# Performance work log

Measured on AMD Instinct MI355X. Metric: run time of the kernel, lower is better.

## Reference

```python
import jax, jax.numpy as jnp
import numpy as np

N_NODES = 50000
N_EDGES = 800000
D = 64
NEG_SLOPE = 0.2


def setup_inputs() -> dict:
    key = jax.random.key(0)
    ks = jax.random.split(key, 16)
    inp = {
        "t": jnp.zeros((1,), jnp.float32),
        "x": jax.random.normal(ks[0], (N_NODES, D), jnp.float32),
        "edge_index": jax.random.randint(ks[1], (2, N_EDGES), 0, N_NODES, jnp.int64),
    }
    # 3 GATConv layers (64->64, 64->64, 64->64), heads=1
    s = 1.0 / np.sqrt(D)
    for li, k0 in zip((1, 2, 3), (2, 6, 10)):
        inp[f"W{li}"] = jax.random.normal(ks[k0], (D, D), jnp.float32) * s
        inp[f"a_src{li}"] = jax.random.normal(ks[k0 + 1], (D,), jnp.float32) * s
        inp[f"a_dst{li}"] = jax.random.normal(ks[k0 + 2], (D,), jnp.float32) * s
        inp[f"b{li}"] = jnp.zeros((D,), jnp.float32)
    return inp


def _gat_conv(x, src, dst, W, a_src, a_dst, b):
    # h = W x  (PyG: lin(x)), per-edge attention, segment softmax over dst
    n = x.shape[0]
    h = x @ W                                   # [N, D]
    score = jax.nn.leaky_relu(h[src] @ a_src + h[dst] @ a_dst, NEG_SLOPE)  # [E]
    smax = jax.ops.segment_max(score, dst, num_segments=n)                 # [N]
    ex = jnp.exp(score - smax[dst])                                        # [E]
    denom = jax.ops.segment_sum(ex, dst, num_segments=n)                   # [N]
    alpha = ex / denom[dst]                                                # [E]
    out = jax.ops.segment_sum(alpha[:, None] * h[src], dst, num_segments=n)
    return out + b


def reference(t, x, edge_index, W1, a_src1, a_dst1, b1, W2, a_src2, a_dst2, b2, W3, a_src3, a_dst3, b3):
    n = x.shape[0]
    # PyG GATConv default add_self_loops=True
    loops = jnp.arange(n, dtype=edge_index.dtype)
    src = jnp.concatenate([edge_index[0], loops])
    dst = jnp.concatenate([edge_index[1], loops])
    h = _gat_conv(x, src, dst, W1, a_src1, a_dst1, b1)
    h = jax.nn.relu(h)
    h = _gat_conv(h, src, dst, W2, a_src2, a_dst2, b2)
    h = jax.nn.relu(h)
    h = _gat_conv(h, src, dst, W3, a_src3, a_dst3, b3)
    return h
```

## Files before the change

kernel.cpp:

```cpp
#include <hip/hip_runtime.h>
#include <hip/hip_fp16.h>

#define NN 50000
#define NE 800000
#define D 64
#define GB ((NN + 63) / 64)
#define NBUCK ((NN + 127) >> 7)
#define CHUNK 4096
#define EBLKS ((NE + CHUNK - 1) / CHUNK)
#define CAPB 4096

__device__ __forceinline__ float lrelu(float s) { return (s > 0.0f) ? s : 0.2f * s; }


__global__ __launch_bounds__(256) void bin_pass(const int* __restrict__ ei,
                                                int* __restrict__ gcur,
                                                unsigned* __restrict__ pairs) {
  __shared__ int cnt_loc[NBUCK];
  __shared__ int base_loc[NBUCK];
  int t = threadIdx.x;
  int e0 = blockIdx.x * CHUNK;
  int n = (NE - e0 < CHUNK) ? (NE - e0) : CHUNK;
  for (int i = t; i < NBUCK; i += 256) cnt_loc[i] = 0;
  __syncthreads();
  for (int i = t; i < n; i += 256)
    atomicAdd(&cnt_loc[ei[NE + e0 + i] >> 7], 1);
  __syncthreads();
  for (int i = t; i < NBUCK; i += 256) {
    int c = cnt_loc[i];
    base_loc[i] = c ? (i * CAPB + atomicAdd(&gcur[i], c)) : 0;
    cnt_loc[i] = 0;
  }
  __syncthreads();
  for (int i = t; i < n; i += 256) {
    int src = ei[e0 + i];
    int dst = ei[NE + e0 + i];
    int b = dst >> 7;
    int off = atomicAdd(&cnt_loc[b], 1);
    unsigned pk = ((unsigned)src << 7) | (unsigned)(dst & 127);
    __builtin_nontemporal_store(pk, &pairs[base_loc[b] + off]);
  }
}

__global__ __launch_bounds__(256) void bucket_sort(const unsigned* __restrict__ pairs,
                                                   const int* __restrict__ gcur,
                                                   int* __restrict__ row_start,
                                                   int* __restrict__ deg,
                                                   int* __restrict__ sorted_src) {
  __shared__ int cnt[128];
  __shared__ int exc[128];
  __shared__ int cur[128];
  __shared__ int buf[CAPB];
  int b = blockIdx.x;
  int t = threadIdx.x;
  int n0 = b << 7;
  int start = b * CAPB;
  int cntb = gcur[b];
  if (cntb > CAPB) cntb = CAPB;
  if (t < 128) cnt[t] = 0;
  __syncthreads();
  for (int i = t; i < cntb; i += 256)
    atomicAdd(&cnt[pairs[start + i] & 127u], 1);
  __syncthreads();
  if (t < 128) exc[t] = cnt[t];
  __syncthreads();
  for (int s = 1; s < 128; s <<= 1) {
    int add = 0;
    if (t < 128 && t >= s) add = exc[t - s];
    __syncthreads();
    if (t < 128) exc[t] += add;
    __syncthreads();
  }
  if (t < 128) {
    int e = exc[t] - cnt[t];
    cur[t] = e;
    int nd = n0 + t;
    if (nd < NN) {
      row_start[nd] = start + e;
      deg[nd] = cnt[t];
    }
  }
  __syncthreads();
  for (int i = t; i < cntb; i += 256) {
    unsigned pk = pairs[start + i];
    int pos = atomicAdd(&cur[pk & 127u], 1);
    if (pos < CAPB) buf[pos] = (int)(pk >> 7);
  }
  __syncthreads();
  for (int i = t; i < cntb; i += 256)
    sorted_src[start + i] = buf[i];
}


__global__ __launch_bounds__(256) void gemm_feat(
    const float* __restrict__ xin, const float* __restrict__ W,
    const float* __restrict__ a_src, const float* __restrict__ a_dst,
    __half* __restrict__ h16, float* __restrict__ s_src, float* __restrict__ s_dst,
    int do_relu) {
  __shared__ float wlds[64 * 64];
  __shared__ float xT[64][68];
  __shared__ float psrc[64][17];
  __shared__ float pdst[64][17];
  int t = threadIdx.x;
  int n0 = blockIdx.x * 64;

  const float4* W4 = (const float4*)W;
  float4* wl4 = (float4*)wlds;
#pragma unroll
  for (int i = 0; i < 4; ++i) wl4[t + 256 * i] = W4[t + 256 * i];

#pragma unroll
  for (int i = 0; i < 4; ++i) {
    int idx = t + 256 * i;
    int r = idx >> 4, c4 = idx & 15;
    int n = n0 + r;
    float4 v = make_float4(0.f, 0.f, 0.f, 0.f);
    if (n < NN) v = ((const float4*)xin)[(size_t)n * 16 + c4];
    if (do_relu) {
      v.x = fmaxf(v.x, 0.f); v.y = fmaxf(v.y, 0.f);
      v.z = fmaxf(v.z, 0.f); v.w = fmaxf(v.w, 0.f);
    }
    xT[c4 * 4 + 0][r] = v.x;
    xT[c4 * 4 + 1][r] = v.y;
    xT[c4 * 4 + 2][r] = v.z;
    xT[c4 * 4 + 3][r] = v.w;
  }
  __syncthreads();

  int tr = t & 15, tc = t >> 4;
  float acc[4][4] = {};
#pragma unroll 8
  for (int k = 0; k < 64; ++k) {
    float4 xa = *(const float4*)&xT[k][tr * 4];
    float4 wv = *(const float4*)&wlds[k * 64 + tc * 4];
    float xs[4] = {xa.x, xa.y, xa.z, xa.w};
    float wj[4] = {wv.x, wv.y, wv.z, wv.w};
#pragma unroll
    for (int i = 0; i < 4; ++i)
#pragma unroll
      for (int j = 0; j < 4; ++j) acc[i][j] = fmaf(xs[i], wj[j], acc[i][j]);
  }

#pragma unroll
  for (int i = 0; i < 4; ++i) {
    int n = n0 + tr * 4 + i;
    if (n < NN) {
      __half2* dst = (__half2*)&h16[(size_t)n * 64 + tc * 4];
      dst[0] = __floats2half2_rn(acc[i][0], acc[i][1]);
      dst[1] = __floats2half2_rn(acc[i][2], acc[i][3]);
    }
  }

  float as[4], ad[4];
#pragma unroll
  for (int j = 0; j < 4; ++j) { as[j] = a_src[tc * 4 + j]; ad[j] = a_dst[tc * 4 + j]; }
#pragma unroll
  for (int i = 0; i < 4; ++i) {
    float p1 = 0.f, p2 = 0.f;
#pragma unroll
    for (int j = 0; j < 4; ++j) { p1 = fmaf(acc[i][j], as[j], p1); p2 = fmaf(acc[i][j], ad[j], p2); }
    psrc[tr * 4 + i][tc] = p1;
    pdst[tr * 4 + i][tc] = p2;
  }
  __syncthreads();
  if (t < 64) {
    int n = n0 + t;
    if (n < NN) {
      float s1 = 0.f, s2 = 0.f;
#pragma unroll
      for (int c = 0; c < 16; ++c) { s1 += psrc[t][c]; s2 += pdst[t][c]; }
      s_src[n] = s1;
      s_dst[n] = s2;
    }
  }
}

__global__ void agg_kernel(const int* __restrict__ sorted_src, const int* __restrict__ row_start,
                           const int* __restrict__ deg, const float* __restrict__ s_src,
                           const float* __restrict__ s_dst, const __half* __restrict__ h16,
                           const float* __restrict__ bias, float* __restrict__ out) {
  int gid = blockIdx.x * blockDim.x + threadIdx.x;
  int n = gid >> 5;
  if (n >= NN) return;
  int lane = threadIdx.x & 31;
  int start = row_start[n];
  int dg = deg[n];
  float sdn = s_dst[n];
  float sself = lrelu(s_src[n] + sdn);
  float exself = __expf(sself - 8.0f);

  float2 acc;
  {
    float2 f = __half22float2(*(const __half2*)&h16[(size_t)n * 64 + 2 * lane]);
    acc.x = exself * f.x;
    acc.y = exself * f.y;
  }
  float dpart = 0.0f;
  for (int base = 0; base < dg; base += 32) {
    int i = base + lane;
    bool act = (i < dg);
    int msrc = act ? __builtin_nontemporal_load(&sorted_src[start + i]) : 0;
    float s = act ? lrelu(s_src[msrc] + sdn) : -INFINITY;
    float ex = __expf(s - 8.0f);
    dpart += ex;
    int nch = (dg - base < 32) ? (dg - base) : 32;
    for (int b0 = 0; b0 < nch; b0 += 8) {
      float xs[8]; int ss[8]; unsigned vv[8];
#pragma unroll
      for (int e = 0; e < 8; ++e) {
        xs[e] = __shfl(ex, b0 + e, 32);
        ss[e] = __shfl(msrc, b0 + e, 32);
      }
#pragma unroll
      for (int e = 0; e < 8; ++e)
        vv[e] = *(const unsigned*)&h16[(size_t)ss[e] * 64 + 2 * lane];
#pragma unroll
      for (int e = 0; e < 8; ++e) {
        float2 f = __half22float2(*(__half2*)&vv[e]);
        acc.x = fmaf(xs[e], f.x, acc.x);
        acc.y = fmaf(xs[e], f.y, acc.y);
      }
    }
  }
#pragma unroll
  for (int off = 16; off > 0; off >>= 1)
    dpart += __shfl_xor(dpart, off, 32);
  float d = exself + dpart;
  float2 bv = *(const float2*)&bias[2 * lane];
  float2 o;
  o.x = acc.x / d + bv.x;
  o.y = acc.y / d + bv.y;
  *(float2*)&out[(size_t)n * 64 + 2 * lane] = o;
}


static void run_layer(const float* xin, int do_relu, const float* W, const float* a_src,
                      const float* a_dst, const float* b, const int* sorted_src,
                      const int* row_start, const int* deg, __half* h16, float* s_src,
                      float* s_dst, float* out, hipStream_t stream) {
  gemm_feat<<<GB, 256, 0, stream>>>(xin, W, a_src, a_dst, h16, s_src, s_dst, do_relu);
  agg_kernel<<<(NN * 32 + 255) / 256, 256, 0, stream>>>(sorted_src, row_start, deg, s_src,
                                                        s_dst, h16, b, out);
}

extern "C" void kernel_launch(void* const* d_in, const int* in_sizes, int n_in,
                              void* d_out, int out_size, void* d_ws, size_t ws_size,
                              hipStream_t stream) {
  const float* x  = (const float*)d_in[1];
  const int*   ei = (const int*)d_in[2];
  const float* W1 = (const float*)d_in[3];
  const float* as1 = (const float*)d_in[4];
  const float* ad1 = (const float*)d_in[5];
  const float* b1 = (const float*)d_in[6];
  const float* W2 = (const float*)d_in[7];
  const float* as2 = (const float*)d_in[8];
  const float* ad2 = (const float*)d_in[9];
  const float* b2 = (const float*)d_in[10];
  const float* W3 = (const float*)d_in[11];
  const float* as3 = (const float*)d_in[12];
  const float* ad3 = (const float*)d_in[13];
  const float* b3 = (const float*)d_in[14];
  float* out = (float*)d_out;

  const size_t ND = (size_t)NN * D;
  char* base = (char*)d_ws;
  __half* h16    = (__half*)base;
  float* A       = (float*)(base + ND * 2);
  float* B       = A + ND;
  float* s_src   = B + ND;
  float* s_dst   = s_src + NN;
  int* row_start = (int*)(s_dst + NN);
  int* deg       = row_start + NN;
  int* gcur      = deg + NN;
  int* sorted_src= gcur + NBUCK;
  unsigned* pairs = (unsigned*)A;

  hipMemsetAsync(gcur, 0, (size_t)NBUCK * sizeof(int), stream);
  bin_pass<<<EBLKS, 256, 0, stream>>>(ei, gcur, pairs);
  bucket_sort<<<NBUCK, 256, 0, stream>>>(pairs, gcur, row_start, deg, sorted_src);

  run_layer(x, 0, W1, as1, ad1, b1, sorted_src, row_start, deg, h16, s_src, s_dst, A, stream);
  run_layer(A, 1, W2, as2, ad2, b2, sorted_src, row_start, deg, h16, s_src, s_dst, B, stream);
  run_layer(B, 1, W3, as3, ad3, b3, sorted_src, row_start, deg, h16, s_src, s_dst, out, stream);
}
```

Measured before the change: 161.5 us.

## Merge binning with first-layer GEMM and pack edge index with half weight

```diff
diff --git a/kernel.cpp b/kernel.cpp
--- a/kernel.cpp
+++ b/kernel.cpp
@@ -13,13 +13,12 @@
 __device__ __forceinline__ float lrelu(float s) { return (s > 0.0f) ? s : 0.2f * s; }
 
 
-__global__ __launch_bounds__(256) void bin_pass(const int* __restrict__ ei,
-                                                int* __restrict__ gcur,
-                                                unsigned* __restrict__ pairs) {
-  __shared__ int cnt_loc[NBUCK];
-  __shared__ int base_loc[NBUCK];
+__device__ __forceinline__ void bin_pass_body(int blk, const int* __restrict__ ei,
+                                              int* __restrict__ gcur,
+                                              unsigned* __restrict__ pairs,
+                                              int* cnt_loc, int* base_loc) {
   int t = threadIdx.x;
-  int e0 = blockIdx.x * CHUNK;
+  int e0 = blk * CHUNK;
   int n = (NE - e0 < CHUNK) ? (NE - e0) : CHUNK;
   for (int i = t; i < NBUCK; i += 256) cnt_loc[i] = 0;
   __syncthreads();
@@ -40,6 +39,122 @@
     unsigned pk = ((unsigned)src << 7) | (unsigned)(dst & 127);
     __builtin_nontemporal_store(pk, &pairs[base_loc[b] + off]);
   }
+}
+
+__device__ __forceinline__ void gemm_body(int gblk, const float* __restrict__ xin,
+                                          const float* __restrict__ W,
+                                          const float* __restrict__ a_src,
+                                          const float* __restrict__ a_dst,
+                                          __half* __restrict__ h16,
+                                          float* __restrict__ s_src,
+                                          float* __restrict__ s_dst, int do_relu,
+                                          float* wlds, float (*xT)[68],
+                                          float (*psrc)[17], float (*pdst)[17]) {
+  int t = threadIdx.x;
+  int n0 = gblk * 64;
+
+  const float4* W4 = (const float4*)W;
+  float4* wl4 = (float4*)wlds;
+#pragma unroll
+  for (int i = 0; i < 4; ++i) wl4[t + 256 * i] = W4[t + 256 * i];
+
+#pragma unroll
+  for (int i = 0; i < 4; ++i) {
+    int idx = t + 256 * i;
+    int r = idx >> 4, c4 = idx & 15;
+    int n = n0 + r;
+    float4 v = make_float4(0.f, 0.f, 0.f, 0.f);
+    if (n < NN) v = ((const float4*)xin)[(size_t)n * 16 + c4];
+    if (do_relu) {
+      v.x = fmaxf(v.x, 0.f); v.y = fmaxf(v.y, 0.f);
+      v.z = fmaxf(v.z, 0.f); v.w = fmaxf(v.w, 0.f);
+    }
+    xT[c4 * 4 + 0][r] = v.x;
+    xT[c4 * 4 + 1][r] = v.y;
+    xT[c4 * 4 + 2][r] = v.z;
+    xT[c4 * 4 + 3][r] = v.w;
+  }
+  __syncthreads();
+
+  int tr = t & 15, tc = t >> 4;
+  float acc[4][4] = {};
+#pragma unroll 8
+  for (int k = 0; k < 64; ++k) {
+    float4 xa = *(const float4*)&xT[k][tr * 4];
+    float4 wv = *(const float4*)&wlds[k * 64 + tc * 4];
+    float xs[4] = {xa.x, xa.y, xa.z, xa.w};
+    float wj[4] = {wv.x, wv.y, wv.z, wv.w};
+#pragma unroll
+    for (int i = 0; i < 4; ++i)
+#pragma unroll
+      for (int j = 0; j < 4; ++j) acc[i][j] = fmaf(xs[i], wj[j], acc[i][j]);
+  }
+
+#pragma unroll
+  for (int i = 0; i < 4; ++i) {
+    int n = n0 + tr * 4 + i;
+    if (n < NN) {
+      __half2* dst = (__half2*)&h16[(size_t)n * 64 + tc * 4];
+      dst[0] = __floats2half2_rn(acc[i][0], acc[i][1]);
+      dst[1] = __floats2half2_rn(acc[i][2], acc[i][3]);
+    }
+  }
+
+  float as[4], ad[4];
+#pragma unroll
+  for (int j = 0; j < 4; ++j) { as[j] = a_src[tc * 4 + j]; ad[j] = a_dst[tc * 4 + j]; }
+#pragma unroll
+  for (int i = 0; i < 4; ++i) {
+    float p1 = 0.f, p2 = 0.f;
+#pragma unroll
+    for (int j = 0; j < 4; ++j) { p1 = fmaf(acc[i][j], as[j], p1); p2 = fmaf(acc[i][j], ad[j], p2); }
+    psrc[tr * 4 + i][tc] = p1;
+    pdst[tr * 4 + i][tc] = p2;
+  }
+  __syncthreads();
+  if (t < 64) {
+    int n = n0 + t;
+    if (n < NN) {
+      float s1 = 0.f, s2 = 0.f;
+#pragma unroll
+      for (int c = 0; c < 16; ++c) { s1 += psrc[t][c]; s2 += pdst[t][c]; }
+      s_src[n] = s1;
+      s_dst[n] = s2;
+    }
+  }
+}
+
+
+__global__ __launch_bounds__(256) void bin_gemm1(
+    const int* __restrict__ ei, int* __restrict__ gcur, unsigned* __restrict__ pairs,
+    const float* __restrict__ xin, const float* __restrict__ W,
+    const float* __restrict__ a_src, const float* __restrict__ a_dst,
+    __half* __restrict__ h16, float* __restrict__ s_src, float* __restrict__ s_dst) {
+  __shared__ float wlds[64 * 64];
+  __shared__ float xT[64][68];
+  __shared__ float psrc[64][17];
+  __shared__ float pdst[64][17];
+  __shared__ int cnt_loc[NBUCK];
+  __shared__ int base_loc[NBUCK];
+  if (blockIdx.x < EBLKS) {
+    bin_pass_body(blockIdx.x, ei, gcur, pairs, cnt_loc, base_loc);
+  } else {
+    gemm_body(blockIdx.x - EBLKS, xin, W, a_src, a_dst, h16, s_src, s_dst, 0,
+              wlds, xT, psrc, pdst);
+  }
+}
+
+__global__ __launch_bounds__(256) void gemm_feat(
+    const float* __restrict__ xin, const float* __restrict__ W,
+    const float* __restrict__ a_src, const float* __restrict__ a_dst,
+    __half* __restrict__ h16, float* __restrict__ s_src, float* __restrict__ s_dst,
+    int do_relu) {
+  __shared__ float wlds[64 * 64];
+  __shared__ float xT[64][68];
+  __shared__ float psrc[64][17];
+  __shared__ float pdst[64][17];
+  gemm_body(blockIdx.x, xin, W, a_src, a_dst, h16, s_src, s_dst, do_relu,
+            wlds, xT, psrc, pdst);
 }
 
 __global__ __launch_bounds__(256) void bucket_sort(const unsigned* __restrict__ pairs,
@@ -91,90 +206,6 @@
     sorted_src[start + i] = buf[i];
 }
 
-
-__global__ __launch_bounds__(256) void gemm_feat(
-    const float* __restrict__ xin, const float* __restrict__ W,
-    const float* __restrict__ a_src, const float* __restrict__ a_dst,
-    __half* __restrict__ h16, float* __restrict__ s_src, float* __restrict__ s_dst,
-    int do_relu) {
-  __shared__ float wlds[64 * 64];
-  __shared__ float xT[64][68];
-  __shared__ float psrc[64][17];
-  __shared__ float pdst[64][17];
-  int t = threadIdx.x;
-  int n0 = blockIdx.x * 64;
-
-  const float4* W4 = (const float4*)W;
-  float4* wl4 = (float4*)wlds;
-#pragma unroll
-  for (int i = 0; i < 4; ++i) wl4[t + 256 * i] = W4[t + 256 * i];
-
-#pragma unroll
-  for (int i = 0; i < 4; ++i) {
-    int idx = t + 256 * i;
-    int r = idx >> 4, c4 = idx & 15;
-    int n = n0 + r;
-    float4 v = make_float4(0.f, 0.f, 0.f, 0.f);
-    if (n < NN) v = ((const float4*)xin)[(size_t)n * 16 + c4];
-    if (do_relu) {
-      v.x = fmaxf(v.x, 0.f); v.y = fmaxf(v.y, 0.f);
-      v.z = fmaxf(v.z, 0.f); v.w = fmaxf(v.w, 0.f);
-    }
-    xT[c4 * 4 + 0][r] = v.x;
-    xT[c4 * 4 + 1][r] = v.y;
-    xT[c4 * 4 + 2][r] = v.z;
-    xT[c4 * 4 + 3][r] = v.w;
-  }
-  __syncthreads();
-
-  int tr = t & 15, tc = t >> 4;
-  float acc[4][4] = {};
-#pragma unroll 8
-  for (int k = 0; k < 64; ++k) {
-    float4 xa = *(const float4*)&xT[k][tr * 4];
-    float4 wv = *(const float4*)&wlds[k * 64 + tc * 4];
-    float xs[4] = {xa.x, xa.y, xa.z, xa.w};
-    float wj[4] = {wv.x, wv.y, wv.z, wv.w};
-#pragma unroll
-    for (int i = 0; i < 4; ++i)
-#pragma unroll
-      for (int j = 0; j < 4; ++j) acc[i][j] = fmaf(xs[i], wj[j], acc[i][j]);
-  }
-
-#pragma unroll
-  for (int i = 0; i < 4; ++i) {
-    int n = n0 + tr * 4 + i;
-    if (n < NN) {
-      __half2* dst = (__half2*)&h16[(size_t)n * 64 + tc * 4];
-      dst[0] = __floats2half2_rn(acc[i][0], acc[i][1]);
-      dst[1] = __floats2half2_rn(acc[i][2], acc[i][3]);
-    }
-  }
-
-  float as[4], ad[4];
-#pragma unroll
-  for (int j = 0; j < 4; ++j) { as[j] = a_src[tc * 4 + j]; ad[j] = a_dst[tc * 4 + j]; }
-#pragma unroll
-  for (int i = 0; i < 4; ++i) {
-    float p1 = 0.f, p2 = 0.f;
-#pragma unroll
-    for (int j = 0; j < 4; ++j) { p1 = fmaf(acc[i][j], as[j], p1); p2 = fmaf(acc[i][j], ad[j], p2); }
-    psrc[tr * 4 + i][tc] = p1;
-    pdst[tr * 4 + i][tc] = p2;
-  }
-  __syncthreads();
-  if (t < 64) {
-    int n = n0 + t;
-    if (n < NN) {
-      float s1 = 0.f, s2 = 0.f;
-#pragma unroll
-      for (int c = 0; c < 16; ++c) { s1 += psrc[t][c]; s2 += pdst[t][c]; }
-      s_src[n] = s1;
-      s_dst[n] = s2;
-    }
-  }
-}
-
 __global__ void agg_kernel(const int* __restrict__ sorted_src, const int* __restrict__ row_start,
                            const int* __restrict__ deg, const float* __restrict__ s_src,
                            const float* __restrict__ s_dst, const __half* __restrict__ h16,
@@ -203,22 +234,23 @@
     float s = act ? lrelu(s_src[msrc] + sdn) : -INFINITY;
     float ex = __expf(s - 8.0f);
     dpart += ex;
+    unsigned pk = ((unsigned)msrc << 16) |
+                  (unsigned)__half_as_ushort(__float2half_rn(ex));
     int nch = (dg - base < 32) ? (dg - base) : 32;
     for (int b0 = 0; b0 < nch; b0 += 8) {
-      float xs[8]; int ss[8]; unsigned vv[8];
+      unsigned pu[8]; unsigned vv[8];
+#pragma unroll
+      for (int e = 0; e < 8; ++e)
+        pu[e] = __shfl(pk, b0 + e, 32);
+#pragma unroll
+      for (int e = 0; e < 8; ++e)
+        vv[e] = *(const unsigned*)&h16[(size_t)(pu[e] >> 16) * 64 + 2 * lane];
 #pragma unroll
       for (int e = 0; e < 8; ++e) {
-        xs[e] = __shfl(ex, b0 + e, 32);
-        ss[e] = __shfl(msrc, b0 + e, 32);
-      }
-#pragma unroll
-      for (int e = 0; e < 8; ++e)
-        vv[e] = *(const unsigned*)&h16[(size_t)ss[e] * 64 + 2 * lane];
-#pragma unroll
-      for (int e = 0; e < 8; ++e) {
+        float xf = __half2float(__ushort_as_half((unsigned short)(pu[e] & 0xFFFFu)));
         float2 f = __half22float2(*(__half2*)&vv[e]);
-        acc.x = fmaf(xs[e], f.x, acc.x);
-        acc.y = fmaf(xs[e], f.y, acc.y);
+        acc.x = fmaf(xf, f.x, acc.x);
+        acc.y = fmaf(xf, f.y, acc.y);
       }
     }
   }
@@ -233,15 +265,6 @@
   *(float2*)&out[(size_t)n * 64 + 2 * lane] = o;
 }
 
-
-static void run_layer(const float* xin, int do_relu, const float* W, const float* a_src,
-                      const float* a_dst, const float* b, const int* sorted_src,
-                      const int* row_start, const int* deg, __half* h16, float* s_src,
-                      float* s_dst, float* out, hipStream_t stream) {
-  gemm_feat<<<GB, 256, 0, stream>>>(xin, W, a_src, a_dst, h16, s_src, s_dst, do_relu);
-  agg_kernel<<<(NN * 32 + 255) / 256, 256, 0, stream>>>(sorted_src, row_start, deg, s_src,
-                                                        s_dst, h16, b, out);
-}
 
 extern "C" void kernel_launch(void* const* d_in, const int* in_sizes, int n_in,
                               void* d_out, int out_size, void* d_ws, size_t ws_size,
@@ -275,11 +298,19 @@
   int* sorted_src= gcur + NBUCK;
   unsigned* pairs = (unsigned*)A;
 
+  const int AGG_BLOCKS = (NN * 32 + 255) / 256;
+
   hipMemsetAsync(gcur, 0, (size_t)NBUCK * sizeof(int), stream);
-  bin_pass<<<EBLKS, 256, 0, stream>>>(ei, gcur, pairs);
+  bin_gemm1<<<EBLKS + GB, 256, 0, stream>>>(ei, gcur, pairs, x, W1, as1, ad1,
+                                            h16, s_src, s_dst);
   bucket_sort<<<NBUCK, 256, 0, stream>>>(pairs, gcur, row_start, deg, sorted_src);
 
-  run_layer(x, 0, W1, as1, ad1, b1, sorted_src, row_start, deg, h16, s_src, s_dst, A, stream);
-  run_layer(A, 1, W2, as2, ad2, b2, sorted_src, row_start, deg, h16, s_src, s_dst, B, stream);
-  run_layer(B, 1, W3, as3, ad3, b3, sorted_src, row_start, deg, h16, s_src, s_dst, out, stream);
-}
+  agg_kernel<<<AGG_BLOCKS, 256, 0, stream>>>(sorted_src, row_start, deg, s_src, s_dst,
+                                             h16, b1, A);
+  gemm_feat<<<GB, 256, 0, stream>>>(A, W2, as2, ad2, h16, s_src, s_dst, 1);
+  agg_kernel<<<AGG_BLOCKS, 256, 0, stream>>>(sorted_src, row_start, deg, s_src, s_dst,
+                                             h16, b2, B);
+  gemm_feat<<<GB, 256, 0, stream>>>(B, W3, as3, ad3, h16, s_src, s_dst, 1);
+  agg_kernel<<<AGG_BLOCKS, 256, 0, stream>>>(sorted_src, row_start, deg, s_src, s_dst,
+                                             h16, b3, out);
+}
```

Result: faster. 149.8 us (-7.2%).
